# Kernel optimization log

Hardware: AMD Instinct MI355X
Metric: run time of the kernel (lower is better)

Reference implementation:

```python
import jax, jax.numpy as jnp
import numpy as np

R = 256   # resolution
C = 16    # n_chan
F = 8     # n_freq
N = 262144


def setup_inputs() -> dict:
    key = jax.random.key(0)
    k1, k2 = jax.random.split(key)
    coords = jax.random.uniform(k1, (N, 3), dtype=jnp.float32, minval=-1.0, maxval=1.0)
    grid = jax.random.normal(k2, (3, C * F, R, R), dtype=jnp.float32) * 0.1
    # matches torch init: linspace(0,1,C*F).reshape(-1,C).T.reshape(-1)
    freqs = jnp.linspace(0.0, 1.0, C * F, dtype=jnp.float32).reshape(-1, C).T.reshape(-1)
    return {"coords": coords, "grid": grid, "freqs": freqs}


def _reflect(x, size):
    # PyTorch grid_sample reflection padding, align_corners=True:
    # reflect unnormalized coords about [0, size-1], period 2*(size-1)
    span = size - 1
    m = 2 * span
    r = jnp.abs(x) % m
    return jnp.where(r > span, m - r, r)


def _grid_sample_plane(img, xy):
    # img: (CF, R, R); xy: (Npts, 2) normalized [-1,1], (x indexes W, y indexes H)
    ix = _reflect((xy[:, 0] + 1.0) * 0.5 * (R - 1), R)
    iy = _reflect((xy[:, 1] + 1.0) * 0.5 * (R - 1), R)
    x0f = jnp.floor(ix); y0f = jnp.floor(iy)
    wx = ix - x0f; wy = iy - y0f
    x0 = jnp.clip(x0f.astype(jnp.int32), 0, R - 1)
    x1 = jnp.clip(x0 + 1, 0, R - 1)
    y0 = jnp.clip(y0f.astype(jnp.int32), 0, R - 1)
    y1 = jnp.clip(y0 + 1, 0, R - 1)
    v00 = img[:, y0, x0]  # (CF, Npts)
    v01 = img[:, y0, x1]
    v10 = img[:, y1, x0]
    v11 = img[:, y1, x1]
    return (v00 * (1 - wx) * (1 - wy) + v01 * wx * (1 - wy)
            + v10 * (1 - wx) * wy + v11 * wx * wy)


def reference(coords, grid, freqs):
    n = coords.shape[0]
    # tri-plane sample coords: plane0 (y,z), plane1 (x,z), plane2 (x,y)
    xy = jnp.stack([coords[:, (1, 2)], coords[:, (0, 2)], coords[:, (0, 1)]], 0)  # (3,N,2)
    coefs = jax.vmap(_grid_sample_plane)(grid, xy)          # (3, CF, N)
    coefs = coefs.transpose(2, 1, 0).reshape(n, C, F, 3)    # (N, C, F, 3)
    # get_freqs(): 2**(clamp(freqs,0,1)*log2(R)) - 1
    fr = 2.0 ** (jnp.clip(freqs, 0.0, 1.0) * np.float32(np.log2(R))) - 1.0  # (CF,)
    pts = (coords + 1.0) * 0.5 * (R - 1)                    # (N, 3)
    phase = (jnp.pi / R) * (pts[:, None, None, :] + 0.5) * (fr.reshape(C, F)[None, :, :, None] + 0.5)
    basis = jnp.cos(phase)                                   # (N, C, F, 3)
    # einsum BCFT,BCFT->BCT then sum over T == sum over (F, T)
    return 2.0 * jnp.sum(coefs * basis, axis=(2, 3))         # (N, C)
```

## Files before the change

kernel.cpp:

```cpp
#include <hip/hip_runtime.h>

#define RES   256
#define NCH   128
#define NC    16
#define QG    32
#define NPK   64
#define NBINS 4096
#define TBLK  3072

__device__ __forceinline__ unsigned int f32_to_bf16_rne(float f) {
    unsigned int u = __float_as_uint(f);
    return (u + 0x7FFFu + ((u >> 16) & 1u)) >> 16;
}
__device__ __forceinline__ float bf16_lo(unsigned int w) {
    return __uint_as_float(w << 16);
}
__device__ __forceinline__ float bf16_hi(unsigned int w) {
    return __uint_as_float(w & 0xFFFF0000u);
}
__device__ __forceinline__ float reflectf(float v) {
    float r = fabsf(v);
    r = fmodf(r, 510.0f);
    return (r > 255.0f) ? (510.0f - r) : r;
}
__device__ __forceinline__ unsigned spread3(unsigned v) {
    return (v & 1u) | ((v & 2u) << 2) | ((v & 4u) << 4) | ((v & 8u) << 6);
}
__device__ __forceinline__ int point_cell(const float* __restrict__ coords, int i) {
    const float r0 = reflectf((coords[3 * (size_t)i + 0] + 1.0f) * 127.5f);
    const float r1 = reflectf((coords[3 * (size_t)i + 1] + 1.0f) * 127.5f);
    const float r2 = reflectf((coords[3 * (size_t)i + 2] + 1.0f) * 127.5f);
    const unsigned cx = (unsigned)min(max((int)r0, 0), 255) >> 4;
    const unsigned cy = (unsigned)min(max((int)r1, 0), 255) >> 4;
    const unsigned cz = (unsigned)min(max((int)r2, 0), 255) >> 4;
    return (int)(spread3(cx) | (spread3(cy) << 1) | (spread3(cz) << 2));
}

__global__ __launch_bounds__(256) void fg_transpose_hist(
    const float* __restrict__ in, unsigned int* __restrict__ out,
    const float* __restrict__ coords, unsigned* __restrict__ hist, int n)
{
    __shared__ unsigned int tile[QG / 2][RES + 4];
    const int tid = threadIdx.x;
    const int qg = blockIdx.x;
    const int y  = blockIdx.y;
    const int p  = blockIdx.z;

    {
        const int bid = (p * RES + y) * 4 + qg;
        const int per = (n + TBLK - 1) / TBLK;
        const int s0 = bid * per;
        const int s1 = min(s0 + per, n);
        for (int k = s0 + tid; k < s1; k += 256)
            atomicAdd(&hist[point_cell(coords, k)], 1u);
    }

    const int q0 = qg * QG;
    const float* src = in + (((size_t)p * NCH + q0) * RES + y) * RES;
    #pragma unroll
    for (int it = 0; it < 4; ++it) {
        const int lin = it * 256 + tid;
        const int k   = lin >> 6;
        const int x4  = lin & 63;
        const float4 a = *(const float4*)(src + (size_t)(2 * k + 0) * (RES * RES) + x4 * 4);
        const float4 b = *(const float4*)(src + (size_t)(2 * k + 1) * (RES * RES) + x4 * 4);
        uint4 w;
        w.x = f32_to_bf16_rne(a.x) | (f32_to_bf16_rne(b.x) << 16);
        w.y = f32_to_bf16_rne(a.y) | (f32_to_bf16_rne(b.y) << 16);
        w.z = f32_to_bf16_rne(a.z) | (f32_to_bf16_rne(b.z) << 16);
        w.w = f32_to_bf16_rne(a.w) | (f32_to_bf16_rne(b.w) << 16);
        *(uint4*)&tile[k][x4 * 4] = w;
    }
    __syncthreads();
    unsigned int* dst = out + (((size_t)p * RES + y) * RES) * NPK + (q0 >> 1);
    #pragma unroll
    for (int it = 0; it < 4; ++it) {
        const int lin = it * 256 + tid;
        const int q4 = lin & 3;
        const int x  = lin >> 2;
        uint4 w;
        w.x = tile[4 * q4 + 0][x];
        w.y = tile[4 * q4 + 1][x];
        w.z = tile[4 * q4 + 2][x];
        w.w = tile[4 * q4 + 3][x];
        *(uint4*)&dst[(size_t)x * NPK + q4 * 4] = w;
    }
}

__global__ __launch_bounds__(256) void fg_scan(
    const unsigned* __restrict__ hist, unsigned* __restrict__ cursor,
    const float* __restrict__ freqs, float* __restrict__ frp)
{
    __shared__ unsigned wtot[4];
    const int t = threadIdx.x;
    const int lane = t & 63;
    const int wid = t >> 6;
    unsigned loc[16];
    unsigned sum = 0;
    #pragma unroll
    for (int k = 0; k < 16; ++k) { loc[k] = hist[t * 16 + k]; sum += loc[k]; }
    unsigned v = sum;
    #pragma unroll
    for (int off = 1; off < 64; off <<= 1) {
        unsigned u = __shfl_up(v, off);
        if (lane >= off) v += u;
    }
    if (lane == 63) wtot[wid] = v;
    __syncthreads();
    unsigned base = 0;
    #pragma unroll
    for (int w = 0; w < 4; ++w) base += (w < wid) ? wtot[w] : 0u;
    unsigned run = base + (v - sum);
    #pragma unroll
    for (int k = 0; k < 16; ++k) { cursor[t * 16 + k] = run; run += loc[k]; }
    if (t < 128) {
        const float f = fminf(fmaxf(freqs[t], 0.0f), 1.0f);
        frp[t] = __builtin_amdgcn_exp2f(f * 8.0f) - 0.5f;
    }
}

__global__ __launch_bounds__(256) void fg_scatter(
    const float* __restrict__ coords, unsigned* __restrict__ cursor,
    unsigned* __restrict__ perm, int n)
{
    const int i = blockIdx.x * 256 + threadIdx.x;
    if (i >= n) return;
    const unsigned pos = atomicAdd(&cursor[point_cell(coords, i)], 1u);
    perm[pos] = (unsigned)i;
}

__global__ __launch_bounds__(256) void fg_main_bf16(
    const float* __restrict__ coords,
    const unsigned int* __restrict__ grid,
    const float* __restrict__ frp_in,
    const unsigned* __restrict__ perm,
    float* __restrict__ out, int n)
{
    const int t = threadIdx.x;
    const int c = t & 15;
    int b = blockIdx.x;
    {
        const int G = gridDim.x;
        const int chunk = G >> 3;
        const int lim = chunk << 3;
        if (b < lim) b = (b & 7) * chunk + (b >> 3);
    }
    const int slot = b * 16 + (t >> 4);
    if (slot >= n) return;
    const int i = (int)perm[slot];

    float frp[8];
    *(float4*)(frp + 0) = *(const float4*)(frp_in + c * 8 + 0);
    *(float4*)(frp + 4) = *(const float4*)(frp_in + c * 8 + 4);

    const float c0 = coords[3 * (size_t)i + 0];
    const float c1 = coords[3 * (size_t)i + 1];
    const float c2 = coords[3 * (size_t)i + 2];
    const float pts0 = (c0 + 1.0f) * 127.5f;
    const float pts1 = (c1 + 1.0f) * 127.5f;
    const float pts2 = (c2 + 1.0f) * 127.5f;

    float acc = 0.0f;

    #pragma unroll
    for (int p = 0; p < 3; ++p) {
        const float sx = (p == 0) ? pts1 : pts0;
        const float sy = (p == 2) ? pts1 : pts2;
        const float pp = (p == 0) ? pts0 : ((p == 1) ? pts1 : pts2);

        const float ix = reflectf(sx);
        const float iy = reflectf(sy);
        const float x0f = floorf(ix), y0f = floorf(iy);
        const float wx = ix - x0f, wy = iy - y0f;
        int x0 = (int)x0f; x0 = min(max(x0, 0), RES - 1);
        int y0 = (int)y0f; y0 = min(max(y0, 0), RES - 1);
        const int x1 = min(x0 + 1, RES - 1);
        const int y1 = min(y0 + 1, RES - 1);
        const float w00 = (1.0f - wx) * (1.0f - wy);
        const float w01 = wx * (1.0f - wy);
        const float w10 = (1.0f - wx) * wy;
        const float w11 = wx * wy;
        const float A = (pp + 0.5f) * (1.0f / 512.0f);

        const size_t rowbase = ((size_t)p * RES) * RES;
        const unsigned int* b00 = grid + (rowbase + (size_t)y0 * RES + x0) * NPK + c * 4;
        const unsigned int* b01 = grid + (rowbase + (size_t)y0 * RES + x1) * NPK + c * 4;
        const unsigned int* b10 = grid + (rowbase + (size_t)y1 * RES + x0) * NPK + c * 4;
        const unsigned int* b11 = grid + (rowbase + (size_t)y1 * RES + x1) * NPK + c * 4;
        const uint4 g00 = *(const uint4*)b00;
        const uint4 g01 = *(const uint4*)b01;
        const uint4 g10 = *(const uint4*)b10;
        const uint4 g11 = *(const uint4*)b11;
        const unsigned int w0[4] = {g00.x, g00.y, g00.z, g00.w};
        const unsigned int w1[4] = {g01.x, g01.y, g01.z, g01.w};
        const unsigned int w2[4] = {g10.x, g10.y, g10.z, g10.w};
        const unsigned int w3[4] = {g11.x, g11.y, g11.z, g11.w};

        #pragma unroll
        for (int jj = 0; jj < 4; ++jj) {
            const float clo = w00 * bf16_lo(w0[jj]) + w01 * bf16_lo(w1[jj])
                            + w10 * bf16_lo(w2[jj]) + w11 * bf16_lo(w3[jj]);
            const float chi = w00 * bf16_hi(w0[jj]) + w01 * bf16_hi(w1[jj])
                            + w10 * bf16_hi(w2[jj]) + w11 * bf16_hi(w3[jj]);
            const float rl = __builtin_amdgcn_fractf(A * frp[2 * jj + 0]);
            const float rh = __builtin_amdgcn_fractf(A * frp[2 * jj + 1]);
            acc += clo * __builtin_amdgcn_cosf(rl);
            acc += chi * __builtin_amdgcn_cosf(rh);
        }
    }

    out[(size_t)i * NC + c] = 2.0f * acc;
}

__global__ __launch_bounds__(256) void fg_main_f32(
    const float* __restrict__ coords,
    const float* __restrict__ grid,
    const float* __restrict__ freqs,
    float* __restrict__ out, int n)
{
    const int t = threadIdx.x;
    const int c = t & 15;
    const int i = blockIdx.x * 16 + (t >> 4);
    if (i >= n) return;

    float frp[8];
    #pragma unroll
    for (int j = 0; j < 8; ++j) {
        float f = fminf(fmaxf(freqs[c * 8 + j], 0.0f), 1.0f);
        frp[j] = __builtin_amdgcn_exp2f(f * 8.0f) - 0.5f;
    }
    const float c0 = coords[3 * (size_t)i + 0];
    const float c1 = coords[3 * (size_t)i + 1];
    const float c2 = coords[3 * (size_t)i + 2];
    const float pts0 = (c0 + 1.0f) * 127.5f;
    const float pts1 = (c1 + 1.0f) * 127.5f;
    const float pts2 = (c2 + 1.0f) * 127.5f;
    float acc = 0.0f;
    #pragma unroll
    for (int p = 0; p < 3; ++p) {
        const float sx = (p == 0) ? pts1 : pts0;
        const float sy = (p == 2) ? pts1 : pts2;
        const float pp = (p == 0) ? pts0 : ((p == 1) ? pts1 : pts2);
        const float ix = reflectf(sx);
        const float iy = reflectf(sy);
        const float x0f = floorf(ix), y0f = floorf(iy);
        const float wx = ix - x0f, wy = iy - y0f;
        int x0 = (int)x0f; x0 = min(max(x0, 0), RES - 1);
        int y0 = (int)y0f; y0 = min(max(y0, 0), RES - 1);
        const int x1 = min(x0 + 1, RES - 1);
        const int y1 = min(y0 + 1, RES - 1);
        const float w00 = (1.0f - wx) * (1.0f - wy);
        const float w01 = wx * (1.0f - wy);
        const float w10 = (1.0f - wx) * wy;
        const float w11 = wx * wy;
        const float A = (pp + 0.5f) * (1.0f / 512.0f);
        const size_t plane = (size_t)p * NCH * RES * RES;
        const int o00 = y0 * RES + x0, o01 = y0 * RES + x1;
        const int o10 = y1 * RES + x0, o11 = y1 * RES + x1;
        #pragma unroll
        for (int j = 0; j < 8; ++j) {
            const float* gq = grid + plane + (size_t)(c * 8 + j) * (RES * RES);
            const float coef = w00 * gq[o00] + w01 * gq[o01]
                             + w10 * gq[o10] + w11 * gq[o11];
            const float rr = __builtin_amdgcn_fractf(A * frp[j]);
            acc += coef * __builtin_amdgcn_cosf(rr);
        }
    }
    out[(size_t)i * NC + c] = 2.0f * acc;
}

extern "C" void kernel_launch(void* const* d_in, const int* in_sizes, int n_in,
                              void* d_out, int out_size, void* d_ws, size_t ws_size,
                              hipStream_t stream)
{
    const float* coords = (const float*)d_in[0];
    const float* grid   = (const float*)d_in[1];
    const float* freqs  = (const float*)d_in[2];
    float* out = (float*)d_out;
    const int n = in_sizes[0] / 3;

    const size_t gridT_b  = (size_t)3 * RES * RES * NPK * sizeof(unsigned);
    const size_t hist_b   = (size_t)NBINS * sizeof(unsigned);
    const size_t frp_b    = 128 * sizeof(float);
    const size_t perm_b   = (size_t)((n + 3) & ~3) * sizeof(unsigned);
    const size_t need = gridT_b + 2 * hist_b + frp_b + perm_b;

    const int blocks = (n + 15) / 16;

    if (ws_size >= need) {
        char* ws = (char*)d_ws;
        unsigned* gridT  = (unsigned*)ws;                 ws += gridT_b;
        unsigned* hist   = (unsigned*)ws;                 ws += hist_b;
        unsigned* cursor = (unsigned*)ws;                 ws += hist_b;
        float*    frp    = (float*)ws;                    ws += frp_b;
        unsigned* perm   = (unsigned*)ws;

        hipMemsetAsync(hist, 0, hist_b, stream);
        hipLaunchKernelGGL(fg_transpose_hist, dim3(4, RES, 3), dim3(256), 0, stream,
                           grid, gridT, coords, hist, n);
        hipLaunchKernelGGL(fg_scan, dim3(1), dim3(256), 0, stream,
                           hist, cursor, freqs, frp);
        hipLaunchKernelGGL(fg_scatter, dim3((n + 255) / 256), dim3(256), 0, stream,
                           coords, cursor, perm, n);
        hipLaunchKernelGGL(fg_main_bf16, dim3(blocks), dim3(256), 0, stream,
                           coords, gridT, frp, perm, out, n);
    } else {
        hipLaunchKernelGGL(fg_main_f32, dim3(blocks), dim3(256), 0, stream,
                           coords, grid, freqs, out, n);
    }
}
```

Baseline: 241.6 us.

## Scatter precomputed point records and batch grid loads in main kernel

The scatter kernel now writes a sorted float4 record holding the scaled coordinates and the original index, so the main kernel reads one contiguous record instead of doing an indirect perm lookup followed by a scattered coords gather. The main kernel issues all twelve grid loads for the three planes before any arithmetic, to expose more memory-level parallelism, and uses 32-bit offsets. Grid reads in the transpose and output stores are marked nontemporal. This costs extra register pressure and a workspace four times larger than the old perm array.

```diff
diff --git a/kernel.cpp b/kernel.cpp
--- a/kernel.cpp
+++ b/kernel.cpp
@@ -7,6 +7,8 @@
 #define NPK   64
 #define NBINS 4096
 #define TBLK  3072
+
+typedef float  fx4 __attribute__((ext_vector_type(4)));
 
 __device__ __forceinline__ unsigned int f32_to_bf16_rne(float f) {
     unsigned int u = __float_as_uint(f);
@@ -62,8 +64,10 @@
         const int lin = it * 256 + tid;
         const int k   = lin >> 6;
         const int x4  = lin & 63;
-        const float4 a = *(const float4*)(src + (size_t)(2 * k + 0) * (RES * RES) + x4 * 4);
-        const float4 b = *(const float4*)(src + (size_t)(2 * k + 1) * (RES * RES) + x4 * 4);
+        const fx4 a = __builtin_nontemporal_load(
+            (const fx4*)(src + (size_t)(2 * k + 0) * (RES * RES) + x4 * 4));
+        const fx4 b = __builtin_nontemporal_load(
+            (const fx4*)(src + (size_t)(2 * k + 1) * (RES * RES) + x4 * 4));
         uint4 w;
         w.x = f32_to_bf16_rne(a.x) | (f32_to_bf16_rne(b.x) << 16);
         w.y = f32_to_bf16_rne(a.y) | (f32_to_bf16_rne(b.y) << 16);
@@ -121,19 +125,31 @@
 
 __global__ __launch_bounds__(256) void fg_scatter(
     const float* __restrict__ coords, unsigned* __restrict__ cursor,
-    unsigned* __restrict__ perm, int n)
+    float4* __restrict__ rec, int n)
 {
     const int i = blockIdx.x * 256 + threadIdx.x;
     if (i >= n) return;
-    const unsigned pos = atomicAdd(&cursor[point_cell(coords, i)], 1u);
-    perm[pos] = (unsigned)i;
+    const float c0 = coords[3 * (size_t)i + 0];
+    const float c1 = coords[3 * (size_t)i + 1];
+    const float c2 = coords[3 * (size_t)i + 2];
+    const float p0 = (c0 + 1.0f) * 127.5f;
+    const float p1 = (c1 + 1.0f) * 127.5f;
+    const float p2 = (c2 + 1.0f) * 127.5f;
+    const float r0 = reflectf(p0);
+    const float r1 = reflectf(p1);
+    const float r2 = reflectf(p2);
+    const unsigned cx = (unsigned)min(max((int)r0, 0), 255) >> 4;
+    const unsigned cy = (unsigned)min(max((int)r1, 0), 255) >> 4;
+    const unsigned cz = (unsigned)min(max((int)r2, 0), 255) >> 4;
+    const int cell = (int)(spread3(cx) | (spread3(cy) << 1) | (spread3(cz) << 2));
+    const unsigned pos = atomicAdd(&cursor[cell], 1u);
+    rec[pos] = make_float4(p0, p1, p2, __uint_as_float((unsigned)i));
 }
 
 __global__ __launch_bounds__(256) void fg_main_bf16(
-    const float* __restrict__ coords,
     const unsigned int* __restrict__ grid,
     const float* __restrict__ frp_in,
-    const unsigned* __restrict__ perm,
+    const float4* __restrict__ rec,
     float* __restrict__ out, int n)
 {
     const int t = threadIdx.x;
@@ -147,20 +163,19 @@
     }
     const int slot = b * 16 + (t >> 4);
     if (slot >= n) return;
-    const int i = (int)perm[slot];
+    const float4 r = rec[slot];
+    const int i = (int)__float_as_uint(r.w);
 
     float frp[8];
     *(float4*)(frp + 0) = *(const float4*)(frp_in + c * 8 + 0);
     *(float4*)(frp + 4) = *(const float4*)(frp_in + c * 8 + 4);
 
-    const float c0 = coords[3 * (size_t)i + 0];
-    const float c1 = coords[3 * (size_t)i + 1];
-    const float c2 = coords[3 * (size_t)i + 2];
-    const float pts0 = (c0 + 1.0f) * 127.5f;
-    const float pts1 = (c1 + 1.0f) * 127.5f;
-    const float pts2 = (c2 + 1.0f) * 127.5f;
-
-    float acc = 0.0f;
+    const float pts0 = r.x;
+    const float pts1 = r.y;
+    const float pts2 = r.z;
+
+    float Aa[3], W00[3], W01[3], W10[3], W11[3];
+    uint4 g[3][4];
 
     #pragma unroll
     for (int p = 0; p < 3; ++p) {
@@ -176,25 +191,32 @@
         int y0 = (int)y0f; y0 = min(max(y0, 0), RES - 1);
         const int x1 = min(x0 + 1, RES - 1);
         const int y1 = min(y0 + 1, RES - 1);
-        const float w00 = (1.0f - wx) * (1.0f - wy);
-        const float w01 = wx * (1.0f - wy);
-        const float w10 = (1.0f - wx) * wy;
-        const float w11 = wx * wy;
-        const float A = (pp + 0.5f) * (1.0f / 512.0f);
-
-        const size_t rowbase = ((size_t)p * RES) * RES;
-        const unsigned int* b00 = grid + (rowbase + (size_t)y0 * RES + x0) * NPK + c * 4;
-        const unsigned int* b01 = grid + (rowbase + (size_t)y0 * RES + x1) * NPK + c * 4;
-        const unsigned int* b10 = grid + (rowbase + (size_t)y1 * RES + x0) * NPK + c * 4;
-        const unsigned int* b11 = grid + (rowbase + (size_t)y1 * RES + x1) * NPK + c * 4;
-        const uint4 g00 = *(const uint4*)b00;
-        const uint4 g01 = *(const uint4*)b01;
-        const uint4 g10 = *(const uint4*)b10;
-        const uint4 g11 = *(const uint4*)b11;
-        const unsigned int w0[4] = {g00.x, g00.y, g00.z, g00.w};
-        const unsigned int w1[4] = {g01.x, g01.y, g01.z, g01.w};
-        const unsigned int w2[4] = {g10.x, g10.y, g10.z, g10.w};
-        const unsigned int w3[4] = {g11.x, g11.y, g11.z, g11.w};
+        W00[p] = (1.0f - wx) * (1.0f - wy);
+        W01[p] = wx * (1.0f - wy);
+        W10[p] = (1.0f - wx) * wy;
+        W11[p] = wx * wy;
+        Aa[p] = (pp + 0.5f) * (1.0f / 512.0f);
+
+        const int rowbase = p * (RES * RES);
+        const int o00 = (rowbase + y0 * RES + x0) * NPK + c * 4;
+        const int o01 = (rowbase + y0 * RES + x1) * NPK + c * 4;
+        const int o10 = (rowbase + y1 * RES + x0) * NPK + c * 4;
+        const int o11 = (rowbase + y1 * RES + x1) * NPK + c * 4;
+        g[p][0] = *(const uint4*)(grid + o00);
+        g[p][1] = *(const uint4*)(grid + o01);
+        g[p][2] = *(const uint4*)(grid + o10);
+        g[p][3] = *(const uint4*)(grid + o11);
+    }
+
+    float acc = 0.0f;
+    #pragma unroll
+    for (int p = 0; p < 3; ++p) {
+        const unsigned int w0[4] = {g[p][0].x, g[p][0].y, g[p][0].z, g[p][0].w};
+        const unsigned int w1[4] = {g[p][1].x, g[p][1].y, g[p][1].z, g[p][1].w};
+        const unsigned int w2[4] = {g[p][2].x, g[p][2].y, g[p][2].z, g[p][2].w};
+        const unsigned int w3[4] = {g[p][3].x, g[p][3].y, g[p][3].z, g[p][3].w};
+        const float w00 = W00[p], w01 = W01[p], w10 = W10[p], w11 = W11[p];
+        const float A = Aa[p];
 
         #pragma unroll
         for (int jj = 0; jj < 4; ++jj) {
@@ -209,7 +231,7 @@
         }
     }
 
-    out[(size_t)i * NC + c] = 2.0f * acc;
+    __builtin_nontemporal_store(2.0f * acc, &out[(size_t)i * NC + c]);
 }
 
 __global__ __launch_bounds__(256) void fg_main_f32(
@@ -282,8 +304,8 @@
     const size_t gridT_b  = (size_t)3 * RES * RES * NPK * sizeof(unsigned);
     const size_t hist_b   = (size_t)NBINS * sizeof(unsigned);
     const size_t frp_b    = 128 * sizeof(float);
-    const size_t perm_b   = (size_t)((n + 3) & ~3) * sizeof(unsigned);
-    const size_t need = gridT_b + 2 * hist_b + frp_b + perm_b;
+    const size_t rec_b    = (size_t)n * sizeof(float4);
+    const size_t need = gridT_b + 2 * hist_b + frp_b + rec_b;
 
     const int blocks = (n + 15) / 16;
 
@@ -293,17 +315,17 @@
         unsigned* hist   = (unsigned*)ws;                 ws += hist_b;
         unsigned* cursor = (unsigned*)ws;                 ws += hist_b;
         float*    frp    = (float*)ws;                    ws += frp_b;
-        unsigned* perm   = (unsigned*)ws;
-
-        hipMemsetAsync(hist, 0, hist_b, stream);
+        float4*   rec    = (float4*)ws;
+
+        (void)hipMemsetAsync(hist, 0, hist_b, stream);
         hipLaunchKernelGGL(fg_transpose_hist, dim3(4, RES, 3), dim3(256), 0, stream,
                            grid, gridT, coords, hist, n);
         hipLaunchKernelGGL(fg_scan, dim3(1), dim3(256), 0, stream,
                            hist, cursor, freqs, frp);
         hipLaunchKernelGGL(fg_scatter, dim3((n + 255) / 256), dim3(256), 0, stream,
-                           coords, cursor, perm, n);
+                           coords, cursor, rec, n);
         hipLaunchKernelGGL(fg_main_bf16, dim3(blocks), dim3(256), 0, stream,
-                           coords, gridT, frp, perm, out, n);
+                           gridT, frp, rec, out, n);
     } else {
         hipLaunchKernelGGL(fg_main_f32, dim3(blocks), dim3(256), 0, stream,
                            coords, grid, freqs, out, n);
```

After: 240.1 us (median of 2 runs). Within noise of the previous version (-0.6%).
